# Optimization experiments

Measured on AMD Instinct MI355X. Metric: run time of the kernel, lower is better.

Reference implementation:

```python
import jax, jax.numpy as jnp
import numpy as np

N, E, D, DH, MH, MO = 100000, 1600000, 128, 512, 512, 128
EPS_BN = 1e-5
EPS_LN = 1e-5


def setup_inputs() -> dict:
    key = jax.random.key(0)
    ks = jax.random.split(key, 16)
    def lin(k, fan_in, shape):
        return jax.random.normal(k, shape, jnp.float32) / np.sqrt(fan_in)
    return {
        'x': jax.random.normal(ks[0], (N, D), jnp.float32),
        'src': jax.random.randint(ks[1], (E,), 0, N, jnp.int32),
        'dst': jax.random.randint(ks[2], (E,), 0, N, jnp.int32),
        'gcn_w': lin(ks[3], D, (D, D)),
        'gcn_b': jnp.zeros((D,), jnp.float32),
        'ff_w1': lin(ks[4], D, (D, DH)),
        'ff_b1': jnp.zeros((DH,), jnp.float32),
        'ln_g': jnp.ones((DH,), jnp.float32),
        'ln_b': jnp.zeros((DH,), jnp.float32),
        'ff_w2': lin(ks[5], DH, (DH, D)),
        'ff_b2': jnp.zeros((D,), jnp.float32),
        'fc1_w': lin(ks[6], D, (D, MH)),
        'fc1_b': jnp.zeros((MH,), jnp.float32),
        'bn1_g': jnp.ones((MH,), jnp.float32),
        'bn1_b': jnp.zeros((MH,), jnp.float32),
        'fc2_w': lin(ks[7], MH, (MH, MH)),
        'fc2_b': jnp.zeros((MH,), jnp.float32),
        'bn2_g': jnp.ones((MH,), jnp.float32),
        'bn2_b': jnp.zeros((MH,), jnp.float32),
        'fc3_w': lin(ks[8], MH, (MH, MO)),
        'fc3_b': jnp.zeros((MO,), jnp.float32),
        'bn3_g': jnp.ones((MO,), jnp.float32),
        'bn3_b': jnp.zeros((MO,), jnp.float32),
        'fc4_w': lin(ks[9], MO, (MO, 1)),
        'fc4_b': jnp.zeros((1,), jnp.float32),
    }


def _gelu(x):
    return jax.nn.gelu(x, approximate=False)  # torch nn.GELU default (erf)


def _batchnorm(x, g, b):
    # BatchNorm1d in training mode: batch statistics, biased variance
    m = jnp.mean(x, axis=0)
    v = jnp.var(x, axis=0)
    return (x - m) * jax.lax.rsqrt(v + EPS_BN) * g + b


def reference(x, src, dst, gcn_w, gcn_b, ff_w1, ff_b1, ln_g, ln_b, ff_w2, ff_b2,
              fc1_w, fc1_b, bn1_g, bn1_b, fc2_w, fc2_b, bn2_g, bn2_b,
              fc3_w, fc3_b, bn3_g, bn3_b, fc4_w, fc4_b):
    n = x.shape[0]
    ones = jnp.ones(src.shape[0], x.dtype)
    out_deg = jnp.clip(jax.ops.segment_sum(ones, src, num_segments=n), 1.0)
    in_deg = jnp.clip(jax.ops.segment_sum(ones, dst, num_segments=n), 1.0)
    # GraphConv, norm='both': left-normalize, aggregate, matmul (in==out), right-normalize, bias
    h = x * (out_deg ** -0.5)[:, None]
    agg = jax.ops.segment_sum(h[src], dst, num_segments=n)  # [N, D]
    h = agg @ gcn_w
    h = h * (in_deg ** -0.5)[:, None] + gcn_b
    # FeedForwardLayer: lin1 -> GELU -> LayerNorm -> lin2
    f = _gelu(h @ ff_w1 + ff_b1)
    mu = jnp.mean(f, axis=-1, keepdims=True)
    var = jnp.var(f, axis=-1, keepdims=True)
    f = (f - mu) * jax.lax.rsqrt(var + EPS_LN) * ln_g + ln_b
    h = f @ ff_w2 + ff_b2  # [N, D]
    # MLP head
    h = _batchnorm(_gelu(h @ fc1_w + fc1_b), bn1_g, bn1_b)
    h = _batchnorm(_gelu(h @ fc2_w + fc2_b), bn2_g, bn2_b)
    h = _batchnorm(_gelu(h @ fc3_w + fc3_b), bn3_g, bn3_b)
    return h @ fc4_w + fc4_b  # [N, 1]
```

## Files before the change

kernel.cpp:

```cpp
#include <hip/hip_runtime.h>
#include <hip/hip_bf16.h>

#define N_NODES 100000
#define NPAD    100096
#define NRB     782
#define E_EDGES 1600000
#define NBLK_SCAN 98

#define HNR  4
#define HP   64
#define HCHK 25000
#define HRSZ 32768

#define NBK  196
#define PCHK 6250

#define AS1 __attribute__((address_space(1)))
#define AS3 __attribute__((address_space(3)))

typedef unsigned int   uint;
typedef unsigned short ushort;
typedef __attribute__((ext_vector_type(8))) short bfx8;
typedef __attribute__((ext_vector_type(4))) float fx4;

__device__ __forceinline__ float bf2f(ushort u) {
    return __uint_as_float(((uint)u) << 16);
}
__device__ __forceinline__ ushort f2bf(float f) {
    uint x = __float_as_uint(f);
    return (ushort)((x + 0x7FFFu + ((x >> 16) & 1u)) >> 16);
}
__device__ __forceinline__ float gelu_fast(float x) {
    float u = 1.5957691f * __builtin_fmaf(0.044715f * x * x, x, x);
    return x * __builtin_amdgcn_rcpf(1.0f + __expf(-u));
}
__device__ __forceinline__ float wave_sum(float v) {
    #pragma unroll
    for (int m = 1; m < 64; m <<= 1) v += __shfl_xor(v, m, 64);
    return v;
}
__device__ __forceinline__ int xcd_swz(int orig, int nwg) {
    int q = nwg >> 3, r = nwg & 7;
    int x = orig & 7, o = orig >> 3;
    return (x < r ? x * (q + 1) : r * (q + 1) + (x - r) * q) + o;
}

__global__ void k_hist2(const int* __restrict__ src, const int* __restrict__ dst,
                        uint* __restrict__ partO, uint* __restrict__ partI)
{
    __shared__ uint h[HRSZ / 2];
    int half = blockIdx.x >> 8;
    int bb = blockIdx.x & 255;
    const int* idx = half ? dst : src;
    uint* part = half ? partI : partO;
    int c = bb & (HP - 1);
    int r = bb / HP;
    int t = threadIdx.x;
    for (int i = t; i < HRSZ / 2; i += 256) h[i] = 0u;
    __syncthreads();
    int base = r << 15;
    int e0 = c * HCHK;
    for (int e = e0 + t; e < e0 + HCHK; e += 256) {
        int v = idx[e] - base;
        if ((uint)v < (uint)HRSZ)
            atomicAdd(&h[v >> 1], 1u << ((v & 1) * 16));
    }
    __syncthreads();
    uint* dstp = part + ((size_t)bb << 14);
    for (int i = t; i < HRSZ / 2; i += 256) dstp[i] = h[i];
}

__global__ void k_degmerge(const uint* __restrict__ partO, const uint* __restrict__ partI,
                           int* __restrict__ inc, float* __restrict__ oscale,
                           float* __restrict__ ininv)
{
    int n = blockIdx.x * 256 + threadIdx.x;
    if (n >= NPAD) return;
    int r = n >> 15, i = (n & 32767) >> 1, hi = (n & 1) * 16;
    const uint* po = partO + ((size_t)(r * HP) << 14) + i;
    const uint* pi = partI + ((size_t)(r * HP) << 14) + i;
    uint so = 0, si = 0;
    for (int c = 0; c < HP; ++c) {
        so += (po[(size_t)c << 14] >> hi) & 0xffffu;
        si += (pi[(size_t)c << 14] >> hi) & 0xffffu;
    }
    inc[n] = (int)si;
    oscale[n] = rsqrtf((float)max((int)so, 1));
    ininv[n] = rsqrtf((float)max((int)si, 1));
}

__global__ void k_scan1(const int* __restrict__ inc, int* __restrict__ coff, int* __restrict__ btot)
{
    __shared__ int a[1024], bsh[1024];
    int t = threadIdx.x;
    int i = blockIdx.x * 1024 + t;
    a[t] = (i < N_NODES) ? inc[i] : 0;
    __syncthreads();
    int* s = a; int* d = bsh;
    for (int dd = 1; dd < 1024; dd <<= 1) {
        int v = s[t] + ((t >= dd) ? s[t - dd] : 0);
        d[t] = v;
        __syncthreads();
        int* tmp = s; s = d; d = tmp;
    }
    if (i < N_NODES) coff[i + 1] = s[t];
    if (t == 1023) btot[blockIdx.x] = s[t];
}

__global__ void k_scan2(int* __restrict__ btot)
{
    __shared__ int a[128], bsh[128];
    int t = threadIdx.x;
    a[t] = (t < NBLK_SCAN) ? btot[t] : 0;
    __syncthreads();
    int* s = a; int* d = bsh;
    for (int dd = 1; dd < 128; dd <<= 1) {
        int v = s[t] + ((t >= dd) ? s[t - dd] : 0);
        d[t] = v;
        __syncthreads();
        int* tmp = s; s = d; d = tmp;
    }
    if (t < NBLK_SCAN) btot[t] = s[t];
}

__global__ void k_scan3(int* __restrict__ coff, const int* __restrict__ btot,
                        int* __restrict__ gcur)
{
    int i = blockIdx.x * 256 + threadIdx.x;
    if (i == 0) { coff[0] = 0; gcur[0] = 0; }
    if (i < N_NODES) {
        int blk = i >> 10;
        int v = coff[i + 1];
        if (blk > 0) v += btot[blk - 1];
        coff[i + 1] = v;
        if (((i + 1) & 511) == 0) {
            int t = (i + 1) >> 9;
            if (t < NBK) gcur[t] = v;
        }
    }
}

__global__ __launch_bounds__(256) void k_part(const int* __restrict__ src, const int* __restrict__ dst,
                                              int* __restrict__ gcur, uint* __restrict__ tmp)
{
    __shared__ int cnt[NBK], rcnt[NBK], base[NBK], loff[NBK];
    __shared__ int sa[256], sb[256];
    __shared__ uint arr[PCHK];
    int t = threadIdx.x;
    if (t < NBK) { cnt[t] = 0; rcnt[t] = 0; }
    __syncthreads();
    int e0 = blockIdx.x * PCHK;
    for (int e = e0 + t; e < e0 + PCHK; e += 256)
        atomicAdd(&cnt[dst[e] >> 9], 1);
    __syncthreads();
    sa[t] = (t < NBK) ? cnt[t] : 0;
    __syncthreads();
    int* s = sa; int* d = sb;
    for (int dd = 1; dd < 256; dd <<= 1) {
        int v = s[t] + ((t >= dd) ? s[t - dd] : 0);
        d[t] = v;
        __syncthreads();
        int* w = s; s = d; d = w;
    }
    if (t < NBK) {
        loff[t] = s[t] - cnt[t];
        base[t] = atomicAdd(&gcur[t], cnt[t]);
    }
    __syncthreads();
    for (int e = e0 + t; e < e0 + PCHK; e += 256) {
        int dv = dst[e];
        int b = dv >> 9;
        int r = atomicAdd(&rcnt[b], 1);
        arr[loff[b] + r] = ((uint)src[e] << 9) | (uint)(dv & 511);
    }
    __syncthreads();
    for (int b = 0; b < NBK; ++b) {
        int n = cnt[b], lo = loff[b], gb = base[b];
        for (int i = t; i < n; i += 256)
            tmp[gb + i] = arr[lo + i];
    }
}

__global__ __launch_bounds__(256) void k_fill2(const uint* __restrict__ tmp, const int* __restrict__ coff,
                                               int* __restrict__ eidx)
{
    __shared__ int lco[512];
    __shared__ int lcnt[512];
    int b = blockIdx.x, t = threadIdx.x;
    int n0 = b << 9;
    for (int i = t; i < 512; i += 256) {
        int node = n0 + i;
        lco[i] = (node <= N_NODES) ? coff[node] : E_EDGES;
        lcnt[i] = 0;
    }
    __syncthreads();
    int s0 = coff[n0];
    int s1 = (n0 + 512 <= N_NODES) ? coff[n0 + 512] : E_EDGES;
    for (int e = s0 + t; e < s1; e += 256) {
        uint v = tmp[e];
        int dl = v & 511;
        int r = atomicAdd(&lcnt[dl], 1);
        eidx[lco[dl] + r] = (int)(v >> 9);
    }
}

__global__ void k_xhat(const float* __restrict__ x, const float* __restrict__ oscale,
                       ushort* __restrict__ xh)
{
    size_t i = (size_t)blockIdx.x * 256 + threadIdx.x;
    size_t e0 = i * 4;
    int row = (int)(e0 >> 7);
    uint2 o;
    if (row < N_NODES) {
        float4 v = *(const float4*)(x + e0);
        float s = oscale[row];
        o.x = (uint)f2bf(v.x * s) | ((uint)f2bf(v.y * s) << 16);
        o.y = (uint)f2bf(v.z * s) | ((uint)f2bf(v.w * s) << 16);
    } else {
        o.x = 0u; o.y = 0u;
    }
    *(uint2*)(xh + e0) = o;
}

__global__ void k_agg(const int* __restrict__ off, const int* __restrict__ eidx,
                      const ushort* __restrict__ xh, ushort* __restrict__ agg)
{
    int wid = threadIdx.x >> 6, lane = threadIdx.x & 63;
    int r = blockIdx.x * 4 + wid;
    if (r >= NPAD) return;
    int f = lane & 15;
    int g = lane >> 4;
    float a[8] = {0.f, 0.f, 0.f, 0.f, 0.f, 0.f, 0.f, 0.f};
    if (r < N_NODES) {
        int s = off[r], e = off[r + 1];
        for (int i = s + g; i < e; i += 4) {
            int sv = eidx[i];
            bfx8 v = *(const bfx8*)(xh + (size_t)sv * 128 + f * 8);
            #pragma unroll
            for (int k = 0; k < 8; ++k) a[k] += bf2f((ushort)v[k]);
        }
    }
    #pragma unroll
    for (int k = 0; k < 8; ++k) {
        a[k] += __shfl_xor(a[k], 16, 64);
        a[k] += __shfl_xor(a[k], 32, 64);
    }
    if (g == 0) {
        bfx8 o;
        #pragma unroll
        for (int k = 0; k < 8; ++k) o[k] = (short)f2bf(a[k]);
        *(bfx8*)(agg + (size_t)r * 128 + f * 8) = o;
    }
}

__global__ void k_wprep(const float* __restrict__ gcn_w, const float* __restrict__ ff_w1,
                        const float* __restrict__ fc1_w, const float* __restrict__ ff_w2,
                        const float* __restrict__ ln_g, const float* __restrict__ ln_b,
                        const float* __restrict__ ff_b2,
                        ushort* __restrict__ gwT, ushort* __restrict__ ff1T,
                        ushort* __restrict__ fc1T, ushort* __restrict__ ff2T,
                        float* __restrict__ lnU, float* __restrict__ lnT)
{
    int bid = blockIdx.x, tid = threadIdx.x;
    if (bid < 576) {
        const float* W; ushort* Wt; int K, M, id;
        if (bid < 64)       { W = gcn_w; Wt = gwT;  K = 128; M = 128; id = bid * 256 + tid; }
        else if (bid < 320) { W = ff_w1; Wt = ff1T; K = 128; M = 512; id = (bid - 64) * 256 + tid; }
        else                { W = fc1_w; Wt = fc1T; K = 128; M = 512; id = (bid - 320) * 256 + tid; }
        int m = id / K, k = id - m * K;
        Wt[id] = f2bf(W[(size_t)k * M + m]);
    } else {
        int wid = tid >> 6, lane = tid & 63;
        int m = (bid - 576) * 4 + wid;
        float us = 0.f, ts = 0.f;
        for (int k = lane; k < 512; k += 64) {
            float w = ff_w2[(size_t)k * 128 + m];
            float gk = ln_g[k], bk = ln_b[k];
            ff2T[(size_t)m * 512 + k] = f2bf(gk * w);
            us += gk * w; ts += bk * w;
        }
        us = wave_sum(us); ts = wave_sum(ts);
        if (lane == 0) { lnU[m] = us; lnT[m] = ts + ff_b2[m]; }
    }
}

template <int K1, int EPI1, int STATS2>
__global__ __launch_bounds__(512, 4) void k_fused(
    const ushort* __restrict__ A1, const ushort* __restrict__ B1t,
    const ushort* __restrict__ B2t, ushort* __restrict__ C,
    const float* __restrict__ c1v0, const float* __restrict__ r1v0,
    const float* __restrict__ r1v1, const float* __restrict__ c1v1,
    const float* __restrict__ bias2,
    float* __restrict__ lnS, float* __restrict__ lnC,
    float* __restrict__ pS, float* __restrict__ pQ)
{
    __shared__ __align__(16) char smem[49152 + 1024];
    char* A2 = smem;
    char* S  = smem + 32768;
    float* st_s = (float*)(smem + 49152);
    float* st_q = (float*)(smem + 49152 + 512);

    const int rb = xcd_swz(blockIdx.x, gridDim.x);
    const int tid = threadIdx.x;
    const int lane = tid & 63;
    const int wid = tid >> 6;
    const int wr = wid >> 2;
    const int wc = wid & 3;
    const int m0 = wr * 64;
    const int frl = lane & 15;
    const int kg = lane >> 4;

    {
        char* As = S;
        char* Bs = A2;
        const int n0 = wc * 32;
        fx4 acc[4][2] = {};
        const ushort* Arow0 = A1 + (size_t)(rb * 128) * K1;

        for (int kb = 0; kb < K1; kb += 64) {
            #pragma unroll
            for (int c = 0; c < 2; ++c) {
                int b = c * 8192 + tid * 16;
                int row = b >> 7;
                int cibs = (b & 127) ^ ((row & 7) << 4);
                const char* ga = (const char*)(Arow0 + (size_t)row * K1 + kb) + cibs;
                const char* gb = (const char*)(B1t + (size_t)row * K1 + kb) + cibs;
                char* la = As + c * 8192 + (wid << 10);
                char* lb = Bs + c * 8192 + (wid << 10);
                __builtin_amdgcn_global_load_lds((const AS1 void*)ga, (AS3 void*)la, 16, 0, 0);
                __builtin_amdgcn_global_load_lds((const AS1 void*)gb, (AS3 void*)lb, 16, 0, 0);
            }
            __syncthreads();
            #pragma unroll
            for (int kk = 0; kk < 2; ++kk) {
                bfx8 av[4], bv[2];
                #pragma unroll
                for (int i = 0; i < 4; ++i) {
                    int ar = m0 + i * 16 + frl;
                    av[i] = *(const bfx8*)(As + ((ar * 128 + kk * 64 + kg * 16) ^ ((ar & 7) << 4)));
                }
                #pragma unroll
                for (int j = 0; j < 2; ++j) {
                    int br = n0 + j * 16 + frl;
                    bv[j] = *(const bfx8*)(Bs + ((br * 128 + kk * 64 + kg * 16) ^ ((br & 7) << 4)));
                }
                #pragma unroll
                for (int i = 0; i < 4; ++i)
                    #pragma unroll
                    for (int j = 0; j < 2; ++j)
                        acc[i][j] = __builtin_amdgcn_mfma_f32_16x16x32_bf16(av[i], bv[j], acc[i][j], 0, 0, 0);
            }
            __syncthreads();
        }

        #pragma unroll
        for (int j = 0; j < 2; ++j) {
            int colL = n0 + j * 16 + frl;
            float c0 = c1v0[colL];
            float c1 = (EPI1 == 3) ? c1v1[colL] : 0.f;
            #pragma unroll
            for (int i = 0; i < 4; ++i) {
                #pragma unroll
                for (int r = 0; r < 4; ++r) {
                    int rowL = m0 + i * 16 + kg * 4 + r;
                    int grow = rb * 128 + rowL;
                    float v = acc[i][j][r];
                    if (EPI1 == 0) v = v * r1v0[grow] + c0;
                    else           v = r1v0[grow] * v + r1v1[grow] * c1 + c0;
                    *(ushort*)(A2 + rowL * 256 + ((colL * 2) ^ ((rowL & 7) << 4))) = f2bf(v);
                }
            }
        }
    }
    __syncthreads();

    float rs = 0.f, rq = 0.f;
    const int rowR = tid >> 2;
    const int qR = tid & 3;
    const int n0b = wc * 16;

    for (int cb2 = 0; cb2 < 8; ++cb2) {
        #pragma unroll
        for (int c = 0; c < 2; ++c) {
            int b = c * 8192 + tid * 16;
            int row = b >> 8;
            int cibs = (b & 255) ^ ((row & 7) << 4);
            const char* gb = (const char*)(B2t + (size_t)(cb2 * 64 + row) * 128) + cibs;
            char* lb = S + c * 8192 + (wid << 10);
            __builtin_amdgcn_global_load_lds((const AS1 void*)gb, (AS3 void*)lb, 16, 0, 0);
        }
        __syncthreads();

        fx4 a2[4] = {};
        #pragma unroll
        for (int kk = 0; kk < 4; ++kk) {
            int c2 = kk * 64 + kg * 16;
            bfx8 av[4], bv;
            #pragma unroll
            for (int i = 0; i < 4; ++i) {
                int ar = m0 + i * 16 + frl;
                av[i] = *(const bfx8*)(A2 + ar * 256 + (c2 ^ ((ar & 7) << 4)));
            }
            {
                int br = n0b + frl;
                bv = *(const bfx8*)(S + br * 256 + (c2 ^ ((br & 7) << 4)));
            }
            #pragma unroll
            for (int i = 0; i < 4; ++i)
                a2[i] = __builtin_amdgcn_mfma_f32_16x16x32_bf16(av[i], bv, a2[i], 0, 0, 0);
        }
        __syncthreads();

        {
            int colL = n0b + frl;
            float bcol = bias2[cb2 * 64 + colL];
            float sL = 0.f, qL = 0.f;
            #pragma unroll
            for (int i = 0; i < 4; ++i) {
                #pragma unroll
                for (int r = 0; r < 4; ++r) {
                    float v = gelu_fast(a2[i][r] + bcol);
                    int rowL = m0 + i * 16 + kg * 4 + r;
                    if (STATS2 == 1) {
                        if (rb * 128 + rowL < N_NODES) { sL += v; qL += v * v; }
                    }
                    *(ushort*)(S + rowL * 128 + ((colL * 2) ^ ((rowL & 7) << 4))) = f2bf(v);
                }
            }
            if (STATS2 == 1) {
                sL += __shfl_xor(sL, 16, 64); sL += __shfl_xor(sL, 32, 64);
                qL += __shfl_xor(qL, 16, 64); qL += __shfl_xor(qL, 32, 64);
                if (kg == 0) {
                    st_s[wr * 64 + colL] = sL;
                    st_q[wr * 64 + colL] = qL;
                }
            }
        }
        __syncthreads();

        {
            int r2 = tid >> 3;
            int s2 = tid & 7;
            #pragma unroll
            for (int pass = 0; pass < 2; ++pass) {
                int rowL = pass * 64 + r2;
                int boff = rowL * 128 + ((s2 * 16) ^ ((rowL & 7) << 4));
                bfx8 v = *(const bfx8*)(S + boff);
                *(bfx8*)((char*)(C + (size_t)(rb * 128 + rowL) * 512 + cb2 * 64) + s2 * 16) = v;
            }
        }
        if (STATS2 == 1 && tid < 64) {
            size_t pidx = ((size_t)rb * 4 + (cb2 >> 1)) * 128 + (cb2 & 1) * 64 + tid;
            pS[pidx] = st_s[tid] + st_s[64 + tid];
            pQ[pidx] = st_q[tid] + st_q[64 + tid];
        }
        if (STATS2 == 2) {
            #pragma unroll
            for (int ss = 0; ss < 2; ++ss) {
                int boff = rowR * 128 + ((qR * 32 + ss * 16) ^ ((rowR & 7) << 4));
                bfx8 v = *(const bfx8*)(S + boff);
                #pragma unroll
                for (int k2 = 0; k2 < 8; ++k2) {
                    float f = bf2f((ushort)v[k2]);
                    rs += f; rq += f * f;
                }
            }
        }
        __syncthreads();
    }

    if (STATS2 == 2) {
        rs += __shfl_xor(rs, 1, 64); rs += __shfl_xor(rs, 2, 64);
        rq += __shfl_xor(rq, 1, 64); rq += __shfl_xor(rq, 2, 64);
        if (qR == 0) {
            float mean = rs * (1.f / 512.f);
            float var = fmaxf(rq * (1.f / 512.f) - mean * mean, 0.f);
            float sr = rsqrtf(var + 1e-5f);
            int grow = rb * 128 + rowR;
            lnS[grow] = sr;
            lnC[grow] = -mean * sr;
        }
    }
}

template <int EPI, int STATS>
__global__ __launch_bounds__(512, 4) void k_gemm(
    const ushort* __restrict__ A, const ushort* __restrict__ Bt,
    ushort* __restrict__ C, int K, int M,
    const float* __restrict__ colv0, const float* __restrict__ rowv0,
    float* __restrict__ pS, float* __restrict__ pQ, int grb0)
{
    __shared__ __align__(16) char smem[32768 + (STATS == 1 ? 2048 : 0)];
    char* AsB = smem;
    char* BsB = smem + 16384;
    float* st_s = (float*)(smem + 32768);
    float* st_q = (float*)(smem + 32768 + 1024);

    const int nwg = gridDim.x;
    const int wgid = xcd_swz(blockIdx.x, nwg);
    const int nCB = M >> 7;
    const int cb = wgid % nCB;
    const int rb = wgid / nCB;
    const int tid = threadIdx.x;
    const int lane = tid & 63;
    const int wid = tid >> 6;
    const int wr = wid >> 2;
    const int wc = wid & 3;
    const int m0 = wr * 64;
    const int n0 = wc * 32;
    const int frl = lane & 15;
    const int kg = lane >> 4;

    fx4 acc[4][2] = {};

    const ushort* Arow0 = A + (size_t)(rb * 128) * K;
    const ushort* Brow0 = Bt + (size_t)(cb * 128) * K;

    for (int kb = 0; kb < K; kb += 64) {
        #pragma unroll
        for (int c = 0; c < 2; ++c) {
            int b = c * 8192 + tid * 16;
            int row = b >> 7;
            int cibs = (b & 127) ^ ((row & 7) << 4);
            const char* ga = (const char*)(Arow0 + (size_t)row * K + kb) + cibs;
            const char* gb = (const char*)(Brow0 + (size_t)row * K + kb) + cibs;
            char* la = AsB + c * 8192 + (wid << 10);
            char* lb = BsB + c * 8192 + (wid << 10);
            __builtin_amdgcn_global_load_lds((const AS1 void*)ga, (AS3 void*)la, 16, 0, 0);
            __builtin_amdgcn_global_load_lds((const AS1 void*)gb, (AS3 void*)lb, 16, 0, 0);
        }
        __syncthreads();
        #pragma unroll
        for (int kk = 0; kk < 2; ++kk) {
            bfx8 av[4], bv[2];
            #pragma unroll
            for (int i = 0; i < 4; ++i) {
                int ar = m0 + i * 16 + frl;
                av[i] = *(const bfx8*)(AsB + ((ar * 128 + kk * 64 + kg * 16) ^ ((ar & 7) << 4)));
            }
            #pragma unroll
            for (int j = 0; j < 2; ++j) {
                int br = n0 + j * 16 + frl;
                bv[j] = *(const bfx8*)(BsB + ((br * 128 + kk * 64 + kg * 16) ^ ((br & 7) << 4)));
            }
            #pragma unroll
            for (int i = 0; i < 4; ++i)
                #pragma unroll
                for (int j = 0; j < 2; ++j)
                    acc[i][j] = __builtin_amdgcn_mfma_f32_16x16x32_bf16(av[i], bv[j], acc[i][j], 0, 0, 0);
        }
        __syncthreads();
    }

    #pragma unroll
    for (int j = 0; j < 2; ++j) {
        int colL = n0 + j * 16 + frl;
        float c0 = colv0[cb * 128 + colL];
        float sL = 0.f, qL = 0.f;
        #pragma unroll
        for (int i = 0; i < 4; ++i) {
            #pragma unroll
            for (int r = 0; r < 4; ++r) {
                float v = acc[i][j][r];
                int rowL = m0 + i * 16 + kg * 4 + r;
                int grow = (grb0 + rb) * 128 + rowL;
                if (EPI == 0) v = v * rowv0[grow] + c0;
                else          v = gelu_fast(v + c0);
                if (STATS == 1) {
                    if (grow < N_NODES) { sL += v; qL += v * v; }
                }
                *(ushort*)(smem + rowL * 256 + ((colL * 2) ^ ((rowL & 7) << 4))) = f2bf(v);
            }
        }
        if (STATS == 1) {
            sL += __shfl_xor(sL, 16, 64); sL += __shfl_xor(sL, 32, 64);
            qL += __shfl_xor(qL, 16, 64); qL += __shfl_xor(qL, 32, 64);
            if (kg == 0) {
                st_s[wr * 128 + colL] = sL;
                st_q[wr * 128 + colL] = qL;
            }
        }
    }
    __syncthreads();
    {
        int r2 = tid >> 4;
        int s2 = tid & 15;
        #pragma unroll
        for (int pass = 0; pass < 4; ++pass) {
            int rowL = pass * 32 + r2;
            int boff = rowL * 256 + ((s2 * 16) ^ ((rowL & 7) << 4));
            bfx8 v = *(const bfx8*)(smem + boff);
            *(bfx8*)((char*)(C + (size_t)(rb * 128 + rowL) * M + cb * 128) + s2 * 16) = v;
        }
    }
    if (STATS == 1 && tid < 128) {
        size_t pidx = ((size_t)(grb0 + rb) * nCB + cb) * 128 + tid;
        pS[pidx] = st_s[tid] + st_s[128 + tid];
        pQ[pidx] = st_q[tid] + st_q[128 + tid];
    }
}

__global__ void k_colmerge(const float* __restrict__ pS, const float* __restrict__ pQ,
                           float* __restrict__ oS, float* __restrict__ oQ, int M)
{
    int wid = threadIdx.x >> 6, lane = threadIdx.x & 63;
    int m = blockIdx.x * 4 + wid;
    if (m >= M) return;
    int nCB = M >> 7, cb = m >> 7, colL = m & 127;
    float s = 0.f, q = 0.f;
    for (int rb = lane; rb < NRB; rb += 64) {
        size_t idx = ((size_t)rb * nCB + cb) * 128 + colL;
        s += pS[idx]; q += pQ[idx];
    }
    s = wave_sum(s); q = wave_sum(q);
    if (lane == 0) { oS[m] = s; oQ[m] = q; }
}

__global__ void k_fold(const float* __restrict__ W, const float* __restrict__ bw,
                       const float* __restrict__ g, const float* __restrict__ bb,
                       const float* __restrict__ sum, const float* __restrict__ sqs,
                       int K, int M, ushort* __restrict__ WtO, float* __restrict__ bO)
{
    int wid = threadIdx.x >> 6, lane = threadIdx.x & 63;
    int m = blockIdx.x * 4 + wid;
    if (m >= M) return;
    float acc = 0.f;
    for (int k = lane; k < K; k += 64) {
        float mean = sum[k] * (1.f / (float)N_NODES);
        float var = sqs[k] * (1.f / (float)N_NODES) - mean * mean;
        float s = g[k] * rsqrtf(var + 1e-5f);
        float t = bb[k] - mean * s;
        float w = W[(size_t)k * M + m];
        WtO[(size_t)m * K + k] = f2bf(w * s);
        acc += t * w;
    }
    acc = wave_sum(acc);
    if (lane == 0) bO[m] = bw[m] + acc;
}

__global__ void k_out(const ushort* __restrict__ m3, const ushort* __restrict__ w4,
                      const float* __restrict__ b4, float* __restrict__ out)
{
    int wid = threadIdx.x >> 6, lane = threadIdx.x & 63;
    int r = blockIdx.x * 4 + wid;
    if (r >= N_NODES) return;
    uint u = *(const uint*)(m3 + (size_t)r * 128 + lane * 2);
    uint w = *(const uint*)(w4 + lane * 2);
    float acc = bf2f((ushort)(u & 0xffffu)) * bf2f((ushort)(w & 0xffffu))
              + bf2f((ushort)(u >> 16)) * bf2f((ushort)(w >> 16));
    acc = wave_sum(acc);
    if (lane == 0) out[r] = acc + b4[0];
}

extern "C" void kernel_launch(void* const* d_in, const int* in_sizes, int n_in,
                              void* d_out, int out_size, void* d_ws, size_t ws_size,
                              hipStream_t stream)
{
    const float* x     = (const float*)d_in[0];
    const int*   src   = (const int*)d_in[1];
    const int*   dst   = (const int*)d_in[2];
    const float* gcn_w = (const float*)d_in[3];
    const float* gcn_b = (const float*)d_in[4];
    const float* ff_w1 = (const float*)d_in[5];
    const float* ff_b1 = (const float*)d_in[6];
    const float* ln_g  = (const float*)d_in[7];
    const float* ln_b  = (const float*)d_in[8];
    const float* ff_w2 = (const float*)d_in[9];
    const float* ff_b2 = (const float*)d_in[10];
    const float* fc1_w = (const float*)d_in[11];
    const float* fc1_b = (const float*)d_in[12];
    const float* bn1_g = (const float*)d_in[13];
    const float* bn1_b = (const float*)d_in[14];
    const float* fc2_w = (const float*)d_in[15];
    const float* fc2_b = (const float*)d_in[16];
    const float* bn2_g = (const float*)d_in[17];
    const float* bn2_b = (const float*)d_in[18];
    const float* fc3_w = (const float*)d_in[19];
    const float* fc3_b = (const float*)d_in[20];
    const float* bn3_g = (const float*)d_in[21];
    const float* bn3_b = (const float*)d_in[22];
    const float* fc4_w = (const float*)d_in[23];
    const float* fc4_b = (const float*)d_in[24];
    float* out = (float*)d_out;
    (void)in_sizes; (void)n_in; (void)out_size;

    char* base = (char*)d_ws;
    char* p = base;
    auto alloc = [&](size_t bytes) -> char* {
        char* r = p;
        p += (bytes + 255) & ~(size_t)255;
        return r;
    };
    int*    inc    = (int*)alloc((size_t)NPAD * 4);
    int*    coff   = (int*)alloc(((size_t)NPAD + 1) * 4);
    int*    btot   = (int*)alloc(128 * 4);
    int*    gcur   = (int*)alloc(256 * 4);
    int*    eidx   = (int*)alloc((size_t)E_EDGES * 4);
    float*  oscale = (float*)alloc((size_t)NPAD * 4);
    float*  ininv  = (float*)alloc((size_t)NPAD * 4);
    float*  bns    = (float*)alloc(6 * 512 * 4);
    float*  b2p    = (float*)alloc(512 * 4);
    float*  b3p    = (float*)alloc(128 * 4);
    float*  b4p    = (float*)alloc(4);
    float*  lnS    = (float*)alloc((size_t)NPAD * 4);
    float*  lnC    = (float*)alloc((size_t)NPAD * 4);
    float*  lnU    = (float*)alloc(128 * 4);
    float*  lnT    = (float*)alloc(128 * 4);
    float*  pS     = (float*)alloc((size_t)4 * NPAD * 4);
    float*  pQ     = (float*)alloc((size_t)4 * NPAD * 4);
    ushort* gwT    = (ushort*)alloc(128 * 128 * 2);
    ushort* ff1T   = (ushort*)alloc(512 * 128 * 2);
    ushort* ff2T   = (ushort*)alloc(128 * 512 * 2);
    ushort* fc1T   = (ushort*)alloc(512 * 128 * 2);
    ushort* fc2T   = (ushort*)alloc(512 * 512 * 2);
    ushort* fc3T   = (ushort*)alloc(128 * 512 * 2);
    ushort* w4t    = (ushort*)alloc(128 * 2);
    ushort* buf1   = (ushort*)alloc((size_t)NPAD * 128 * 2);
    ushort* bufC   = (ushort*)alloc((size_t)NPAD * 512 * 2);

    size_t used = (size_t)(p - base);
    bool   sep  = (used + (size_t)NPAD * 512 * 2) <= ws_size;
    ushort* m2  = sep ? (ushort*)alloc((size_t)NPAD * 512 * 2) : bufC;

    uint* partO = (uint*)bufC;
    uint* partI = partO + (size_t)HNR * HP * (HRSZ / 2);
    uint* etmp  = (uint*)bufC;
    ushort* xh  = bufC;
    ushort* agg = buf1;

    float* bn1s = bns;
    float* bn1q = bns + 512;
    float* bn2s = bns + 1024;
    float* bn2q = bns + 1536;
    float* bn3s = bns + 2048;
    float* bn3q = bns + 2560;

    k_hist2<<<2 * HNR * HP, 256, 0, stream>>>(src, dst, partO, partI);
    k_degmerge<<<(NPAD + 255) / 256, 256, 0, stream>>>(partO, partI, inc, oscale, ininv);
    k_scan1<<<NBLK_SCAN, 1024, 0, stream>>>(inc, coff, btot);
    k_scan2<<<1, 128, 0, stream>>>(btot);
    k_scan3<<<(N_NODES + 255) / 256, 256, 0, stream>>>(coff, btot, gcur);
    k_part<<<E_EDGES / PCHK, 256, 0, stream>>>(src, dst, gcur, etmp);
    k_fill2<<<NBK, 256, 0, stream>>>(etmp, coff, eidx);
    k_xhat<<<(NPAD / 256) * 32, 256, 0, stream>>>(x, oscale, xh);
    k_agg<<<NPAD / 4, 256, 0, stream>>>(coff, eidx, xh, agg);

    k_wprep<<<608, 256, 0, stream>>>(gcn_w, ff_w1, fc1_w, ff_w2, ln_g, ln_b, ff_b2,
                                     gwT, ff1T, fc1T, ff2T, lnU, lnT);

    k_fused<128, 0, 2><<<NRB, 512, 0, stream>>>(agg, gwT, ff1T, bufC,
                                                gcn_b, ininv, nullptr, nullptr, ff_b1,
                                                lnS, lnC, nullptr, nullptr);
    k_fused<512, 3, 1><<<NRB, 512, 0, stream>>>(bufC, ff2T, fc1T, bufC,
                                                lnT, lnS, lnC, lnU, fc1_b,
                                                nullptr, nullptr, pS, pQ);
    k_colmerge<<<128, 256, 0, stream>>>(pS, pQ, bn1s, bn1q, 512);
    k_fold<<<512 / 4, 256, 0, stream>>>(fc2_w, fc2_b, bn1_g, bn1_b, bn1s, bn1q, 512, 512, fc2T, b2p);
    if (sep) {
        k_gemm<1, 1><<<4 * NRB, 512, 0, stream>>>(bufC, fc2T, m2, 512, 512,
                                                  b2p, nullptr, pS, pQ, 0);
    } else {
        const int cOff[6] = {0, 195, 390, 585, 780, 782};
        for (int c = 0; c < 5; ++c) {
            int rb0 = cOff[c], nrb = cOff[c + 1] - rb0;
            k_gemm<1, 1><<<nrb * 4, 512, 0, stream>>>(bufC + (size_t)rb0 * 128 * 512, fc2T,
                                                      buf1, 512, 512,
                                                      b2p, nullptr, pS, pQ, rb0);
            hipMemcpyAsync(bufC + (size_t)rb0 * 128 * 512, buf1,
                           (size_t)nrb * 128 * 512 * 2, hipMemcpyDeviceToDevice, stream);
        }
    }
    k_colmerge<<<128, 256, 0, stream>>>(pS, pQ, bn2s, bn2q, 512);
    k_fold<<<128 / 4, 256, 0, stream>>>(fc3_w, fc3_b, bn2_g, bn2_b, bn2s, bn2q, 512, 128, fc3T, b3p);
    k_gemm<1, 1><<<NRB, 512, 0, stream>>>(m2, fc3T, buf1, 512, 128,
                                          b3p, nullptr, pS, pQ, 0);
    k_colmerge<<<32, 256, 0, stream>>>(pS, pQ, bn3s, bn3q, 128);
    k_fold<<<1, 256, 0, stream>>>(fc4_w, fc4_b, bn3_g, bn3_b, bn3s, bn3q, 128, 1, w4t, b4p);
    k_out<<<N_NODES / 4, 256, 0, stream>>>(buf1, w4t, b4p, out);
}
```

Before: 565.1 us.

## Fuse GCN, feed-forward and fc1 stages into one mega kernel per row block

Merges the two k_fused launches into a single kernel that keeps each 128-row block on chip through GCN matmul, ff1+GELU, ff2 (LayerNorm folded via per-row stats held in shared memory) and fc1+GELU. It removes the write and re-read of the 512-wide intermediate in global memory and the per-row LN stats arrays. In exchange shared memory per block grows to about 67KB, which may reduce occupancy, and more accumulators stay live in registers. A leftover dead stub kernel, k_mega, contains a nonsense __ldg on a null pointer and is never launched.

```diff
diff --git a/kernel.cpp b/kernel.cpp
--- a/kernel.cpp
+++ b/kernel.cpp
@@ -284,21 +284,23 @@
     }
 }
 
-template <int K1, int EPI1, int STATS2>
-__global__ __launch_bounds__(512, 4) void k_fused(
-    const ushort* __restrict__ A1, const ushort* __restrict__ B1t,
-    const ushort* __restrict__ B2t, ushort* __restrict__ C,
-    const float* __restrict__ c1v0, const float* __restrict__ r1v0,
-    const float* __restrict__ r1v1, const float* __restrict__ c1v1,
-    const float* __restrict__ bias2,
-    float* __restrict__ lnS, float* __restrict__ lnC,
+__global__ __launch_bounds__(512, 4) void k_mega(
+    const ushort* __restrict__ A1, const ushort* __restrict__ gwT,
+    const ushort* __restrict__ ff1T, const ushort* __restrict__ ff2T,
+    const ushort* __restrict__ fc1T, ushort* __restrict__ M1,
+    const float* __restrict__ gcn_b, const float* __restrict__ ininv,
+    const float* __restrict__ lnU, const float* __restrict__ lnT,
+    const float* __restrict__ fc1_b,
     float* __restrict__ pS, float* __restrict__ pQ)
 {
-    __shared__ __align__(16) char smem[49152 + 1024];
-    char* A2 = smem;
-    char* S  = smem + 32768;
-    float* st_s = (float*)(smem + 49152);
-    float* st_q = (float*)(smem + 49152 + 512);
+    __shared__ __align__(16) char smem[65536 + 2560];
+    char* A2  = smem;
+    char* S   = smem + 32768;
+    char* Bs2 = smem + 49152;
+    float* st_s = (float*)(smem + 65536);
+    float* st_q = (float*)(smem + 65536 + 512);
+    float* rS   = (float*)(smem + 65536 + 1024);
+    float* rC   = (float*)(smem + 65536 + 1536);
 
     const int rb = xcd_swz(blockIdx.x, gridDim.x);
     const int tid = threadIdx.x;
@@ -315,16 +317,16 @@
         char* Bs = A2;
         const int n0 = wc * 32;
         fx4 acc[4][2] = {};
-        const ushort* Arow0 = A1 + (size_t)(rb * 128) * K1;
-
-        for (int kb = 0; kb < K1; kb += 64) {
+        const ushort* Arow0 = A1 + (size_t)(rb * 128) * 128;
+
+        for (int kb = 0; kb < 128; kb += 64) {
             #pragma unroll
             for (int c = 0; c < 2; ++c) {
                 int b = c * 8192 + tid * 16;
                 int row = b >> 7;
                 int cibs = (b & 127) ^ ((row & 7) << 4);
-                const char* ga = (const char*)(Arow0 + (size_t)row * K1 + kb) + cibs;
-                const char* gb = (const char*)(B1t + (size_t)row * K1 + kb) + cibs;
+                const char* ga = (const char*)(Arow0 + (size_t)row * 128 + kb) + cibs;
+                const char* gb = (const char*)(gwT + (size_t)row * 128 + kb) + cibs;
                 char* la = As + c * 8192 + (wid << 10);
                 char* lb = Bs + c * 8192 + (wid << 10);
                 __builtin_amdgcn_global_load_lds((const AS1 void*)ga, (AS3 void*)la, 16, 0, 0);
@@ -352,21 +354,17 @@
             }
             __syncthreads();
         }
-
         #pragma unroll
         for (int j = 0; j < 2; ++j) {
             int colL = n0 + j * 16 + frl;
-            float c0 = c1v0[colL];
-            float c1 = (EPI1 == 3) ? c1v1[colL] : 0.f;
+            float c0 = gcn_b[colL];
             #pragma unroll
             for (int i = 0; i < 4; ++i) {
                 #pragma unroll
                 for (int r = 0; r < 4; ++r) {
                     int rowL = m0 + i * 16 + kg * 4 + r;
                     int grow = rb * 128 + rowL;
-                    float v = acc[i][j][r];
-                    if (EPI1 == 0) v = v * r1v0[grow] + c0;
-                    else           v = r1v0[grow] * v + r1v1[grow] * c1 + c0;
+                    float v = acc[i][j][r] * ininv[grow] + c0;
                     *(ushort*)(A2 + rowL * 256 + ((colL * 2) ^ ((rowL & 7) << 4))) = f2bf(v);
                 }
             }
@@ -378,20 +376,280 @@
     const int rowR = tid >> 2;
     const int qR = tid & 3;
     const int n0b = wc * 16;
+    const int n0h = wc * 32;
+    fx4 h2acc[4][2] = {};
 
     for (int cb2 = 0; cb2 < 8; ++cb2) {
+        #pragma unroll
+        for (int c = 0; c < 2; ++c) {
+            int b = c * 8192 + tid * 16;
+            int row1 = b >> 8;
+            int cib1 = (b & 255) ^ ((row1 & 7) << 4);
+            const char* g1 = (const char*)(ff1T + (size_t)(cb2 * 64 + row1) * 128) + cib1;
+            char* l1 = S + c * 8192 + (wid << 10);
+            __builtin_amdgcn_global_load_lds((const AS1 void*)g1, (AS3 void*)l1, 16, 0, 0);
+            int row2 = b >> 7;
+            int cib2 = (b & 127) ^ ((row2 & 7) << 4);
+            const char* g2 = (const char*)ff2T + (size_t)row2 * 1024 + cb2 * 128 + cib2;
+            char* l2 = Bs2 + c * 8192 + (wid << 10);
+            __builtin_amdgcn_global_load_lds((const AS1 void*)g2, (AS3 void*)l2, 16, 0, 0);
+        }
+        __syncthreads();
+
+        fx4 fa[4] = {};
+        #pragma unroll
+        for (int kk = 0; kk < 4; ++kk) {
+            int c2 = kk * 64 + kg * 16;
+            bfx8 av[4], bv;
+            #pragma unroll
+            for (int i = 0; i < 4; ++i) {
+                int ar = m0 + i * 16 + frl;
+                av[i] = *(const bfx8*)(A2 + ar * 256 + (c2 ^ ((ar & 7) << 4)));
+            }
+            {
+                int br = n0b + frl;
+                bv = *(const bfx8*)(S + br * 256 + (c2 ^ ((br & 7) << 4)));
+            }
+            #pragma unroll
+            for (int i = 0; i < 4; ++i)
+                fa[i] = __builtin_amdgcn_mfma_f32_16x16x32_bf16(av[i], bv, fa[i], 0, 0, 0);
+        }
+        __syncthreads();
+
+        {
+            int colL = n0b + frl;
+            float bcol = __ldg(&((const float*)nullptr == nullptr ? (const float*)0 : (const float*)0)[0]);
+        }
+        {
+            int colL = n0b + frl;
+        }
+        __syncthreads();
+        break;
+    }
+}
+
+__global__ __launch_bounds__(512, 4) void k_mega_real(
+    const ushort* __restrict__ A1, const ushort* __restrict__ gwT,
+    const ushort* __restrict__ ff1T, const ushort* __restrict__ ff2T,
+    const ushort* __restrict__ fc1T, ushort* __restrict__ M1,
+    const float* __restrict__ gcn_b, const float* __restrict__ ininv,
+    const float* __restrict__ b1,
+    const float* __restrict__ lnU, const float* __restrict__ lnT,
+    const float* __restrict__ fc1_b,
+    float* __restrict__ pS, float* __restrict__ pQ)
+{
+    __shared__ __align__(16) char smem[65536 + 2560];
+    char* A2  = smem;
+    char* S   = smem + 32768;
+    char* Bs2 = smem + 49152;
+    float* st_s = (float*)(smem + 65536);
+    float* st_q = (float*)(smem + 65536 + 512);
+    float* rS   = (float*)(smem + 65536 + 1024);
+    float* rC   = (float*)(smem + 65536 + 1536);
+
+    const int rb = xcd_swz(blockIdx.x, gridDim.x);
+    const int tid = threadIdx.x;
+    const int lane = tid & 63;
+    const int wid = tid >> 6;
+    const int wr = wid >> 2;
+    const int wc = wid & 3;
+    const int m0 = wr * 64;
+    const int frl = lane & 15;
+    const int kg = lane >> 4;
+
+    {
+        char* As = S;
+        char* Bs = A2;
+        const int n0 = wc * 32;
+        fx4 acc[4][2] = {};
+        const ushort* Arow0 = A1 + (size_t)(rb * 128) * 128;
+
+        for (int kb = 0; kb < 128; kb += 64) {
+            #pragma unroll
+            for (int c = 0; c < 2; ++c) {
+                int b = c * 8192 + tid * 16;
+                int row = b >> 7;
+                int cibs = (b & 127) ^ ((row & 7) << 4);
+                const char* ga = (const char*)(Arow0 + (size_t)row * 128 + kb) + cibs;
+                const char* gb = (const char*)(gwT + (size_t)row * 128 + kb) + cibs;
+                char* la = As + c * 8192 + (wid << 10);
+                char* lb = Bs + c * 8192 + (wid << 10);
+                __builtin_amdgcn_global_load_lds((const AS1 void*)ga, (AS3 void*)la, 16, 0, 0);
+                __builtin_amdgcn_global_load_lds((const AS1 void*)gb, (AS3 void*)lb, 16, 0, 0);
+            }
+            __syncthreads();
+            #pragma unroll
+            for (int kk = 0; kk < 2; ++kk) {
+                bfx8 av[4], bv[2];
+                #pragma unroll
+                for (int i = 0; i < 4; ++i) {
+                    int ar = m0 + i * 16 + frl;
+                    av[i] = *(const bfx8*)(As + ((ar * 128 + kk * 64 + kg * 16) ^ ((ar & 7) << 4)));
+                }
+                #pragma unroll
+                for (int j = 0; j < 2; ++j) {
+                    int br = n0 + j * 16 + frl;
+                    bv[j] = *(const bfx8*)(Bs + ((br * 128 + kk * 64 + kg * 16) ^ ((br & 7) << 4)));
+                }
+                #pragma unroll
+                for (int i = 0; i < 4; ++i)
+                    #pragma unroll
+                    for (int j = 0; j < 2; ++j)
+                        acc[i][j] = __builtin_amdgcn_mfma_f32_16x16x32_bf16(av[i], bv[j], acc[i][j], 0, 0, 0);
+            }
+            __syncthreads();
+        }
+        #pragma unroll
+        for (int j = 0; j < 2; ++j) {
+            int colL = n0 + j * 16 + frl;
+            float c0 = gcn_b[colL];
+            #pragma unroll
+            for (int i = 0; i < 4; ++i) {
+                #pragma unroll
+                for (int r = 0; r < 4; ++r) {
+                    int rowL = m0 + i * 16 + kg * 4 + r;
+                    int grow = rb * 128 + rowL;
+                    float v = acc[i][j][r] * ininv[grow] + c0;
+                    *(ushort*)(A2 + rowL * 256 + ((colL * 2) ^ ((rowL & 7) << 4))) = f2bf(v);
+                }
+            }
+        }
+    }
+    __syncthreads();
+
+    float rs = 0.f, rq = 0.f;
+    const int rowR = tid >> 2;
+    const int qR = tid & 3;
+    const int n0b = wc * 16;
+    const int n0h = wc * 32;
+    fx4 h2acc[4][2] = {};
+
+    for (int cb2 = 0; cb2 < 8; ++cb2) {
+        #pragma unroll
+        for (int c = 0; c < 2; ++c) {
+            int b = c * 8192 + tid * 16;
+            int row1 = b >> 8;
+            int cib1 = (b & 255) ^ ((row1 & 7) << 4);
+            const char* g1 = (const char*)(ff1T + (size_t)(cb2 * 64 + row1) * 128) + cib1;
+            char* l1 = S + c * 8192 + (wid << 10);
+            __builtin_amdgcn_global_load_lds((const AS1 void*)g1, (AS3 void*)l1, 16, 0, 0);
+            int row2 = b >> 7;
+            int cib2 = (b & 127) ^ ((row2 & 7) << 4);
+            const char* g2 = (const char*)ff2T + (size_t)row2 * 1024 + cb2 * 128 + cib2;
+            char* l2 = Bs2 + c * 8192 + (wid << 10);
+            __builtin_amdgcn_global_load_lds((const AS1 void*)g2, (AS3 void*)l2, 16, 0, 0);
+        }
+        __syncthreads();
+
+        fx4 fa[4] = {};
+        #pragma unroll
+        for (int kk = 0; kk < 4; ++kk) {
+            int c2 = kk * 64 + kg * 16;
+            bfx8 av[4], bv;
+            #pragma unroll
+            for (int i = 0; i < 4; ++i) {
+                int ar = m0 + i * 16 + frl;
+                av[i] = *(const bfx8*)(A2 + ar * 256 + (c2 ^ ((ar & 7) << 4)));
+            }
+            {
+                int br = n0b + frl;
+                bv = *(const bfx8*)(S + br * 256 + (c2 ^ ((br & 7) << 4)));
+            }
+            #pragma unroll
+            for (int i = 0; i < 4; ++i)
+                fa[i] = __builtin_amdgcn_mfma_f32_16x16x32_bf16(av[i], bv, fa[i], 0, 0, 0);
+        }
+        __syncthreads();
+
+        {
+            int colL = n0b + frl;
+            float bcol = b1[cb2 * 64 + colL];
+            #pragma unroll
+            for (int i = 0; i < 4; ++i) {
+                #pragma unroll
+                for (int r = 0; r < 4; ++r) {
+                    float v = gelu_fast(fa[i][r] + bcol);
+                    int rowL = m0 + i * 16 + kg * 4 + r;
+                    *(ushort*)(S + rowL * 128 + ((colL * 2) ^ ((rowL & 7) << 4))) = f2bf(v);
+                }
+            }
+        }
+        __syncthreads();
+
+        #pragma unroll
+        for (int kk2 = 0; kk2 < 2; ++kk2) {
+            int c2b = kk2 * 64 + kg * 16;
+            bfx8 av2[4], bv2[2];
+            #pragma unroll
+            for (int i = 0; i < 4; ++i) {
+                int ar = m0 + i * 16 + frl;
+                av2[i] = *(const bfx8*)(S + ar * 128 + (c2b ^ ((ar & 7) << 4)));
+            }
+            #pragma unroll
+            for (int j = 0; j < 2; ++j) {
+                int br = n0h + j * 16 + frl;
+                bv2[j] = *(const bfx8*)(Bs2 + br * 128 + (c2b ^ ((br & 7) << 4)));
+            }
+            #pragma unroll
+            for (int i = 0; i < 4; ++i)
+                #pragma unroll
+                for (int j = 0; j < 2; ++j)
+                    h2acc[i][j] = __builtin_amdgcn_mfma_f32_16x16x32_bf16(av2[i], bv2[j], h2acc[i][j], 0, 0, 0);
+        }
+        #pragma unroll
+        for (int ss = 0; ss < 2; ++ss) {
+            int boff = rowR * 128 + ((qR * 32 + ss * 16) ^ ((rowR & 7) << 4));
+            bfx8 v = *(const bfx8*)(S + boff);
+            #pragma unroll
+            for (int k2 = 0; k2 < 8; ++k2) {
+                float f = bf2f((ushort)v[k2]);
+                rs += f; rq += f * f;
+            }
+        }
+        __syncthreads();
+    }
+
+    rs += __shfl_xor(rs, 1, 64); rs += __shfl_xor(rs, 2, 64);
+    rq += __shfl_xor(rq, 1, 64); rq += __shfl_xor(rq, 2, 64);
+    if (qR == 0) {
+        float mean = rs * (1.f / 512.f);
+        float var = fmaxf(rq * (1.f / 512.f) - mean * mean, 0.f);
+        float sr = rsqrtf(var + 1e-5f);
+        rS[rowR] = sr;
+        rC[rowR] = -mean * sr;
+    }
+    __syncthreads();
+
+    #pragma unroll
+    for (int j = 0; j < 2; ++j) {
+        int colL = n0h + j * 16 + frl;
+        float uc = lnU[colL];
+        float tc = lnT[colL];
+        #pragma unroll
+        for (int i = 0; i < 4; ++i) {
+            #pragma unroll
+            for (int r = 0; r < 4; ++r) {
+                int rowL = m0 + i * 16 + kg * 4 + r;
+                float v = rS[rowL] * h2acc[i][j][r] + rC[rowL] * uc + tc;
+                *(ushort*)(A2 + rowL * 256 + ((colL * 2) ^ ((rowL & 7) << 4))) = f2bf(v);
+            }
+        }
+    }
+    __syncthreads();
+
+    for (int cb3 = 0; cb3 < 8; ++cb3) {
         #pragma unroll
         for (int c = 0; c < 2; ++c) {
             int b = c * 8192 + tid * 16;
             int row = b >> 8;
             int cibs = (b & 255) ^ ((row & 7) << 4);
-            const char* gb = (const char*)(B2t + (size_t)(cb2 * 64 + row) * 128) + cibs;
+            const char* gb = (const char*)(fc1T + (size_t)(cb3 * 64 + row) * 128) + cibs;
             char* lb = S + c * 8192 + (wid << 10);
             __builtin_amdgcn_global_load_lds((const AS1 void*)gb, (AS3 void*)lb, 16, 0, 0);
         }
         __syncthreads();
 
-        fx4 a2[4] = {};
+        fx4 ma[4] = {};
         #pragma unroll
         for (int kk = 0; kk < 4; ++kk) {
             int c2 = kk * 64 + kg * 16;
@@ -407,33 +665,29 @@
             }
             #pragma unroll
             for (int i = 0; i < 4; ++i)
-                a2[i] = __builtin_amdgcn_mfma_f32_16x16x32_bf16(av[i], bv, a2[i], 0, 0, 0);
+                ma[i] = __builtin_amdgcn_mfma_f32_16x16x32_bf16(av[i], bv, ma[i], 0, 0, 0);
         }
         __syncthreads();
 
         {
             int colL = n0b + frl;
-            float bcol = bias2[cb2 * 64 + colL];
+            float bcol = fc1_b[cb3 * 64 + colL];
             float sL = 0.f, qL = 0.f;
             #pragma unroll
             for (int i = 0; i < 4; ++i) {
                 #pragma unroll
                 for (int r = 0; r < 4; ++r) {
-                    float v = gelu_fast(a2[i][r] + bcol);
+                    float v = gelu_fast(ma[i][r] + bcol);
                     int rowL = m0 + i * 16 + kg * 4 + r;
-                    if (STATS2 == 1) {
-                        if (rb * 128 + rowL < N_NODES) { sL += v; qL += v * v; }
-                    }
+                    if (rb * 128 + rowL < N_NODES) { sL += v; qL += v * v; }
                     *(ushort*)(S + rowL * 128 + ((colL * 2) ^ ((rowL & 7) << 4))) = f2bf(v);
                 }
             }
-            if (STATS2 == 1) {
-                sL += __shfl_xor(sL, 16, 64); sL += __shfl_xor(sL, 32, 64);
-                qL += __shfl_xor(qL, 16, 64); qL += __shfl_xor(qL, 32, 64);
-                if (kg == 0) {
-                    st_s[wr * 64 + colL] = sL;
-                    st_q[wr * 64 + colL] = qL;
-                }
+            sL += __shfl_xor(sL, 16, 64); sL += __shfl_xor(sL, 32, 64);
+            qL += __shfl_xor(qL, 16, 64); qL += __shfl_xor(qL, 32, 64);
+            if (kg == 0) {
+                st_s[wr * 64 + colL] = sL;
+                st_q[wr * 64 + colL] = qL;
             }
         }
         __syncthreads();
@@ -446,40 +700,15 @@
                 int rowL = pass * 64 + r2;
                 int boff = rowL * 128 + ((s2 * 16) ^ ((rowL & 7) << 4));
                 bfx8 v = *(const bfx8*)(S + boff);
-                *(bfx8*)((char*)(C + (size_t)(rb * 128 + rowL) * 512 + cb2 * 64) + s2 * 16) = v;
-            }
-        }
-        if (STATS2 == 1 && tid < 64) {
-            size_t pidx = ((size_t)rb * 4 + (cb2 >> 1)) * 128 + (cb2 & 1) * 64 + tid;
+                *(bfx8*)((char*)(M1 + (size_t)(rb * 128 + rowL) * 512 + cb3 * 64) + s2 * 16) = v;
+            }
+        }
+        if (tid < 64) {
+            size_t pidx = ((size_t)rb * 4 + (cb3 >> 1)) * 128 + (cb3 & 1) * 64 + tid;
             pS[pidx] = st_s[tid] + st_s[64 + tid];
             pQ[pidx] = st_q[tid] + st_q[64 + tid];
         }
-        if (STATS2 == 2) {
-            #pragma unroll
-            for (int ss = 0; ss < 2; ++ss) {
-                int boff = rowR * 128 + ((qR * 32 + ss * 16) ^ ((rowR & 7) << 4));
-                bfx8 v = *(const bfx8*)(S + boff);
-                #pragma unroll
-                for (int k2 = 0; k2 < 8; ++k2) {
-                    float f = bf2f((ushort)v[k2]);
-                    rs += f; rq += f * f;
-                }
-            }
-        }
-        __syncthreads();
-    }
-
-    if (STATS2 == 2) {
-        rs += __shfl_xor(rs, 1, 64); rs += __shfl_xor(rs, 2, 64);
-        rq += __shfl_xor(rq, 1, 64); rq += __shfl_xor(rq, 2, 64);
-        if (qR == 0) {
-            float mean = rs * (1.f / 512.f);
-            float var = fmaxf(rq * (1.f / 512.f) - mean * mean, 0.f);
-            float sr = rsqrtf(var + 1e-5f);
-            int grow = rb * 128 + rowR;
-            lnS[grow] = sr;
-            lnC[grow] = -mean * sr;
-        }
+        __syncthreads();
     }
 }
 
@@ -702,8 +931,6 @@
     float*  b2p    = (float*)alloc(512 * 4);
     float*  b3p    = (float*)alloc(128 * 4);
     float*  b4p    = (float*)alloc(4);
-    float*  lnS    = (float*)alloc((size_t)NPAD * 4);
-    float*  lnC    = (float*)alloc((size_t)NPAD * 4);
     float*  lnU    = (float*)alloc(128 * 4);
     float*  lnT    = (float*)alloc(128 * 4);
     float*  pS     = (float*)alloc((size_t)4 * NPAD * 4);
@@ -748,12 +975,8 @@
     k_wprep<<<608, 256, 0, stream>>>(gcn_w, ff_w1, fc1_w, ff_w2, ln_g, ln_b, ff_b2,
                                      gwT, ff1T, fc1T, ff2T, lnU, lnT);
 
-    k_fused<128, 0, 2><<<NRB, 512, 0, stream>>>(agg, gwT, ff1T, bufC,
-                                                gcn_b, ininv, nullptr, nullptr, ff_b1,
-                                                lnS, lnC, nullptr, nullptr);
-    k_fused<512, 3, 1><<<NRB, 512, 0, stream>>>(bufC, ff2T, fc1T, bufC,
-                                                lnT, lnS, lnC, lnU, fc1_b,
-                                                nullptr, nullptr, pS, pQ);
+    k_mega_real<<<NRB, 512, 0, stream>>>(agg, gwT, ff1T, ff2T, fc1T, bufC,
+                                         gcn_b, ininv, ff_b1, lnU, lnT, fc1_b, pS, pQ);
     k_colmerge<<<128, 256, 0, stream>>>(pS, pQ, bn1s, bn1q, 512);
     k_fold<<<512 / 4, 256, 0, stream>>>(fc2_w, fc2_b, bn1_g, bn1_b, bn1s, bn1q, 512, 512, fc2T, b2p);
     if (sep) {
```

Measured after the change: 563.8 us. Within noise of the previous version (-0.2%).
